# Kernel tuning notes

Hardware: AMD Instinct MI355X
Metric: run time of the kernel (lower is better)

Reference implementation:

```python
import jax, jax.numpy as jnp
import numpy as np

B, T, D, H = 4, 2048, 1024, 16
HD = D // H  # head_dim = 64

def setup_inputs() -> dict:
    key = jax.random.key(0)
    k1, k2, k3 = jax.random.split(key, 3)
    s = 1.0 / np.sqrt(D)
    return {
        "x": jax.random.normal(k1, (B, T, D), dtype=jnp.float32),
        "w_qkv": jax.random.normal(k2, (D, 3 * D), dtype=jnp.float32) * s,
        "b_qkv": jnp.zeros((3 * D,), dtype=jnp.float32),
        "w_proj": jax.random.normal(k3, (D, D), dtype=jnp.float32) * s,
        "b_proj": jnp.zeros((D,), dtype=jnp.float32),
    }

def reference(x, w_qkv, b_qkv, w_proj, b_proj):
    b, t, c = x.shape
    qkv = x @ w_qkv + b_qkv                       # [B,T,3D]
    qkv = qkv.reshape(b, t, 3, H, HD)
    q, k, v = (jnp.transpose(qkv[:, :, i], (0, 2, 1, 3)) for i in range(3))  # [B,H,T,HD]
    scale = 1.0 / np.sqrt(HD)
    attn = jnp.einsum('bhqd,bhkd->bhqk', q, k) * scale  # [B,H,T,T]
    attn = jax.nn.softmax(attn, axis=-1)
    out = jnp.einsum('bhqk,bhkd->bhqd', attn, v)        # [B,H,T,HD]
    out = jnp.transpose(out, (0, 2, 1, 3)).reshape(b, t, c)
    return out @ w_proj + b_proj
```

## Files before the change

### kernel.cpp

```cpp
#include <hip/hip_runtime.h>
#include <hip/hip_bf16.h>

#define T_SEQ   2048
#define D_MODEL 1024
#define N_HEADS 16
#define HEAD_DIM 64
#define BT      8192
#define N3D     3072

using short8  = __attribute__((ext_vector_type(8))) short;
using short4v = __attribute__((ext_vector_type(4))) short;
using floatx4 = __attribute__((ext_vector_type(4))) float;

#define QSCALE 0.18033688f

__device__ __forceinline__ unsigned short rne_bf16(float f) {
  unsigned int u = __float_as_uint(f);
  u = (u + 0x7fffu + ((u >> 16) & 1u)) >> 16;
  return (unsigned short)u;
}

__device__ __forceinline__ void gload_lds16(const unsigned short* g,
                                            unsigned short* l) {
  __builtin_amdgcn_global_load_lds(
      (const __attribute__((address_space(1))) void*)g,
      (__attribute__((address_space(3))) void*)l, 16, 0, 0);
}

__global__ __launch_bounds__(256) void k_convert(const float* __restrict__ in,
                                                 unsigned short* __restrict__ out) {
  size_t i = ((size_t)blockIdx.x * 256 + threadIdx.x) * 8;
  float4 a = *(const float4*)(in + i);
  float4 b = *(const float4*)(in + i + 4);
  short8 v;
  v[0] = (short)rne_bf16(a.x); v[1] = (short)rne_bf16(a.y);
  v[2] = (short)rne_bf16(a.z); v[3] = (short)rne_bf16(a.w);
  v[4] = (short)rne_bf16(b.x); v[5] = (short)rne_bf16(b.y);
  v[6] = (short)rne_bf16(b.z); v[7] = (short)rne_bf16(b.w);
  *(short8*)(((short*)out) + i) = v;
}

__global__ __launch_bounds__(256) void k_transpose_convert(
    const float* __restrict__ in, unsigned short* __restrict__ out_hi,
    int R, int C) {
  __shared__ float tile[64][65];
  int tiles_c = C >> 6;
  int r0 = (blockIdx.x / tiles_c) << 6;
  int c0 = (blockIdx.x % tiles_c) << 6;
  int tid = threadIdx.x;
#pragma unroll
  for (int i = 0; i < 16; ++i) {
    int idx = tid + i * 256;
    int r = idx >> 6, c = idx & 63;
    tile[r][c] = in[(size_t)(r0 + r) * C + c0 + c];
  }
  __syncthreads();
#pragma unroll
  for (int i = 0; i < 16; ++i) {
    int idx = tid + i * 256;
    int orow = idx >> 6, oc = idx & 63;
    out_hi[(size_t)(c0 + orow) * R + r0 + oc] = rne_bf16(tile[oc][orow]);
  }
}

__global__ __launch_bounds__(256) void k_qkv_gemm(
    const unsigned short* __restrict__ A, const unsigned short* __restrict__ Bt,
    const float* __restrict__ bias,
    unsigned short* __restrict__ Qo, unsigned short* __restrict__ Ko,
    unsigned short* __restrict__ Vt) {
  __shared__ __align__(16) unsigned short As[128 * 64];
  __shared__ __align__(16) unsigned short Bs[128 * 64];
  int tid = threadIdx.x;
  int wg = (blockIdx.x & 7) * 192 + (blockIdx.x >> 3);
  int m0 = (wg / 24) * 128;
  int n0 = (wg % 24) * 128;
  int which = n0 >> 10;
  int w = tid >> 6, lane = tid & 63, quad = lane >> 4, l16 = lane & 15;
  int wm = (w >> 1) * 64, wn = (w & 1) * 64;
  floatx4 acc[4][4] = {};

  int r0 = tid >> 3;
  int gsh = (((tid & 7) ^ (r0 & 7)) << 3);

  int a_off[4][2], b_off[4][2];
#pragma unroll
  for (int t = 0; t < 4; ++t) {
    int ra = wm + t * 16 + l16, rb = wn + t * 16 + l16;
#pragma unroll
    for (int ks = 0; ks < 2; ++ks) {
      a_off[t][ks] = ra * 64 + (((ks * 4 + quad) ^ (ra & 7)) << 3);
      b_off[t][ks] = rb * 64 + (((ks * 4 + quad) ^ (rb & 7)) << 3);
    }
  }

  for (int k0 = 0; k0 < 1024; k0 += 64) {
#pragma unroll
    for (int i = 0; i < 4; ++i) {
      int sub = (tid & ~63) + i * 256;
      gload_lds16(A + (size_t)(m0 + r0 + i * 32) * 1024 + k0 + gsh,
                  &As[sub * 8]);
      gload_lds16(Bt + (size_t)(n0 + r0 + i * 32) * 1024 + k0 + gsh,
                  &Bs[sub * 8]);
    }
    __syncthreads();
#pragma unroll
    for (int ks = 0; ks < 2; ++ks) {
      short8 af[4], bfr[4];
#pragma unroll
      for (int mt = 0; mt < 4; ++mt) af[mt] = *(const short8*)(&As[a_off[mt][ks]]);
#pragma unroll
      for (int nt = 0; nt < 4; ++nt) bfr[nt] = *(const short8*)(&Bs[b_off[nt][ks]]);
      if (which == 2) {
#pragma unroll
        for (int mt = 0; mt < 4; ++mt)
#pragma unroll
          for (int nt = 0; nt < 4; ++nt)
            acc[mt][nt] = __builtin_amdgcn_mfma_f32_16x16x32_bf16(af[mt], bfr[nt],
                                                                  acc[mt][nt], 0, 0, 0);
      } else {
#pragma unroll
        for (int mt = 0; mt < 4; ++mt)
#pragma unroll
          for (int nt = 0; nt < 4; ++nt)
            acc[mt][nt] = __builtin_amdgcn_mfma_f32_16x16x32_bf16(bfr[nt], af[mt],
                                                                  acc[mt][nt], 0, 0, 0);
      }
    }
    __syncthreads();
  }

  if (which == 2) {
#pragma unroll
    for (int nt = 0; nt < 4; ++nt) {
      int n = n0 + wn + nt * 16 + l16;
      float bv = bias[n];
      int nn = n & 1023;
      int h = nn >> 6, hd = nn & 63;
#pragma unroll
      for (int mt = 0; mt < 4; ++mt) {
        int mbase = m0 + wm + mt * 16 + quad * 4;
        int b = mbase >> 11;
        int t0 = mbase & 2047;
        int head = b * N_HEADS + h;
        short4v vv;
#pragma unroll
        for (int r = 0; r < 4; ++r) vv[r] = (short)rne_bf16(acc[mt][nt][r] + bv);
        *(short4v*)(&Vt[((size_t)head * HEAD_DIM + hd) * T_SEQ + t0]) = vv;
      }
    }
  } else {
    unsigned short* dst = (which == 0) ? Qo : Ko;
    float scl = (which == 0) ? QSCALE : 1.0f;
#pragma unroll
    for (int nt = 0; nt < 4; ++nt) {
      int nbase = n0 + wn + nt * 16 + quad * 4;
      int nn = nbase & 1023;
      int h = nn >> 6, hd0 = nn & 63;
      float4 bv4 = *(const float4*)(&bias[nbase]);
#pragma unroll
      for (int mt = 0; mt < 4; ++mt) {
        int m = m0 + wm + mt * 16 + l16;
        int b = m >> 11;
        int t = m & 2047;
        int head = b * N_HEADS + h;
        short4v ov;
        ov[0] = (short)rne_bf16((acc[mt][nt][0] + bv4.x) * scl);
        ov[1] = (short)rne_bf16((acc[mt][nt][1] + bv4.y) * scl);
        ov[2] = (short)rne_bf16((acc[mt][nt][2] + bv4.z) * scl);
        ov[3] = (short)rne_bf16((acc[mt][nt][3] + bv4.w) * scl);
        *(short4v*)(&dst[((size_t)head * T_SEQ + t) * HEAD_DIM + hd0]) = ov;
      }
    }
  }
}

__global__ __launch_bounds__(512, 4) void k_attn(
    const unsigned short* __restrict__ Q, const unsigned short* __restrict__ K,
    const unsigned short* __restrict__ Vt, unsigned short* __restrict__ Oo) {
  __shared__ __align__(16) unsigned short Klds[2][64 * 64];
  __shared__ __align__(16) unsigned short Vlds[3][64 * 64];
  int tid = threadIdx.x;
  int head = ((blockIdx.x & 7) << 3) + (blockIdx.x >> 6);
  int qb = ((blockIdx.x >> 3) & 7) << 8;
  int b = head >> 4, h = head & 15;
  int w = tid >> 6, lane = tid & 63, quad = lane >> 4, l16 = lane & 15;
  const unsigned short* Qh = Q + (size_t)head * T_SEQ * HEAD_DIM;
  const unsigned short* Kh = K + (size_t)head * T_SEQ * HEAD_DIM;
  const unsigned short* Vh = Vt + (size_t)head * HEAD_DIM * T_SEQ;

  short8 qf[2][2];
#pragma unroll
  for (int qi = 0; qi < 2; ++qi) {
    int qrow = qb + w * 32 + qi * 16 + l16;
#pragma unroll
    for (int ks = 0; ks < 2; ++ks)
      qf[qi][ks] = *(const short8*)(Qh + (size_t)qrow * 64 + ks * 32 + quad * 8);
  }

  short8 ones;
#pragma unroll
  for (int j = 0; j < 8; ++j) ones[j] = (short)0x3F80;

  floatx4 O[2][4] = {};
  floatx4 Osum[2] = {};
  const floatx4 zf = {};

  int sg = tid >> 6;
  int xs = lane ^ sg;
  int ntp = xs >> 4, mp = xs & 15;
  int ksrc = ((ntp >> 1) << 5) + ((mp >> 2) << 3) + ((ntp & 1) << 2) + (mp & 3);
  int vsrc = xs;
  int sub = tid & ~63;

  int pu[2][4];
#pragma unroll
  for (int ks = 0; ks < 2; ++ks) {
    int gk = ks * 4 + quad;
#pragma unroll
    for (int t = 0; t < 4; ++t)
      pu[ks][t] = (((gk << 6) + t * 16 + l16) ^ gk) << 3;
  }

  auto stageK = [&](unsigned short* dst, int kb) {
    gload_lds16(Kh + ((size_t)(kb * 64 + ksrc)) * 64 + sg * 8, dst + sub * 8);
  };
  auto stageV = [&](unsigned short* dst, int kb) {
    gload_lds16(Vh + (size_t)vsrc * T_SEQ + kb * 64 + sg * 8, dst + sub * 8);
  };

  short8 pPrev[2][2];

  auto qk = [&](const unsigned short* Kb_, floatx4 (&s)[2][4]) {
#pragma unroll
    for (int ks = 0; ks < 2; ++ks) {
#pragma unroll
      for (int nt = 0; nt < 4; ++nt) {
        short8 kf = *(const short8*)(Kb_ + pu[ks][nt]);
        if (ks == 0) {
          s[0][nt] = __builtin_amdgcn_mfma_f32_16x16x32_bf16(kf, qf[0][0], zf, 0, 0, 0);
          s[1][nt] = __builtin_amdgcn_mfma_f32_16x16x32_bf16(kf, qf[1][0], zf, 0, 0, 0);
        } else {
          s[0][nt] = __builtin_amdgcn_mfma_f32_16x16x32_bf16(kf, qf[0][1], s[0][nt], 0, 0, 0);
          s[1][nt] = __builtin_amdgcn_mfma_f32_16x16x32_bf16(kf, qf[1][1], s[1][nt], 0, 0, 0);
        }
      }
    }
  };

  auto pv = [&](const unsigned short* Vb_) {
#pragma unroll
    for (int ks = 0; ks < 2; ++ks) {
      Osum[0] = __builtin_amdgcn_mfma_f32_16x16x32_bf16(ones, pPrev[0][ks], Osum[0], 0, 0, 0);
      Osum[1] = __builtin_amdgcn_mfma_f32_16x16x32_bf16(ones, pPrev[1][ks], Osum[1], 0, 0, 0);
#pragma unroll
      for (int dt = 0; dt < 4; ++dt) {
        short8 vf = *(const short8*)(Vb_ + pu[ks][dt]);
        O[0][dt] = __builtin_amdgcn_mfma_f32_16x16x32_bf16(vf, pPrev[0][ks], O[0][dt], 0, 0, 0);
        O[1][dt] = __builtin_amdgcn_mfma_f32_16x16x32_bf16(vf, pPrev[1][ks], O[1][dt], 0, 0, 0);
      }
    }
  };

  auto expPack = [&](floatx4 (&s)[2][4]) {
#pragma unroll
    for (int qi = 0; qi < 2; ++qi) {
      unsigned int dw[4][2];
#pragma unroll
      for (int nt = 0; nt < 4; ++nt) {
        float p0 = __builtin_amdgcn_exp2f(s[qi][nt][0]);
        float p1 = __builtin_amdgcn_exp2f(s[qi][nt][1]);
        float p2 = __builtin_amdgcn_exp2f(s[qi][nt][2]);
        float p3 = __builtin_amdgcn_exp2f(s[qi][nt][3]);
        __hip_bfloat162 lo2 = __float22bfloat162_rn(make_float2(p0, p1));
        __hip_bfloat162 hi2 = __float22bfloat162_rn(make_float2(p2, p3));
        dw[nt][0] = *(unsigned int*)&lo2;
        dw[nt][1] = *(unsigned int*)&hi2;
      }
#pragma unroll
      for (int ks = 0; ks < 2; ++ks) {
        union { unsigned int u[4]; short8 s8; } cv;
        cv.u[0] = dw[2 * ks][0];
        cv.u[1] = dw[2 * ks][1];
        cv.u[2] = dw[2 * ks + 1][0];
        cv.u[3] = dw[2 * ks + 1][1];
        pPrev[qi][ks] = cv.s8;
      }
    }
  };

  unsigned short* Kcur = &Klds[1][0];
  unsigned short* Koth = &Klds[0][0];
  unsigned short* Vp = &Vlds[0][0];
  unsigned short* Vc = &Vlds[1][0];
  unsigned short* Vn = &Vlds[2][0];

  stageK(Koth, 0); stageV(Vp, 0);
  __syncthreads();
  stageK(Kcur, 1); stageV(Vc, 1);
  {
    floatx4 s[2][4];
    qk(Koth, s);
    expPack(s);
  }
  __syncthreads();

#pragma unroll 1
  for (int t = 1; t < 32; ++t) {
    if (t < 31) { stageK(Koth, t + 1); stageV(Vn, t + 1); }
    floatx4 s[2][4];
    __builtin_amdgcn_s_setprio(1);
    qk(Kcur, s);
    pv(Vp);
    __builtin_amdgcn_s_setprio(0);
    expPack(s);
    __syncthreads();
    unsigned short* tk = Kcur; Kcur = Koth; Koth = tk;
    unsigned short* tv = Vp; Vp = Vc; Vc = Vn; Vn = tv;
  }
  pv(Vp);

#pragma unroll
  for (int qi = 0; qi < 2; ++qi) {
    float inv = 1.0f / Osum[qi][0];
    int t = qb + w * 32 + qi * 16 + l16;
    size_t rowo = ((size_t)(b * T_SEQ + t)) * D_MODEL + h * HEAD_DIM;
#pragma unroll
    for (int dt = 0; dt < 4; ++dt) {
      short4v ov;
#pragma unroll
      for (int r = 0; r < 4; ++r) ov[r] = (short)rne_bf16(O[qi][dt][r] * inv);
      *(short4v*)(&Oo[rowo + dt * 16 + quad * 4]) = ov;
    }
  }
}

__global__ __launch_bounds__(256) void k_proj_gemm(
    const unsigned short* __restrict__ A, const unsigned short* __restrict__ Bt,
    const float* __restrict__ bias, float* __restrict__ out) {
  __shared__ __align__(16) unsigned short As[128 * 64];
  __shared__ __align__(16) unsigned short Bs[128 * 64];
  int tid = threadIdx.x;
  int wg = (blockIdx.x & 7) * 64 + (blockIdx.x >> 3);
  int m0 = (wg >> 3) * 128;
  int n0 = (wg & 7) * 128;
  int w = tid >> 6, lane = tid & 63, quad = lane >> 4, l16 = lane & 15;
  int wm = (w >> 1) * 64, wn = (w & 1) * 64;
  floatx4 acc[4][4] = {};

  int r0 = tid >> 3;
  int gsh = (((tid & 7) ^ (r0 & 7)) << 3);

  int a_off[4][2], b_off[4][2];
#pragma unroll
  for (int t = 0; t < 4; ++t) {
    int ra = wm + t * 16 + l16, rb = wn + t * 16 + l16;
#pragma unroll
    for (int ks = 0; ks < 2; ++ks) {
      a_off[t][ks] = ra * 64 + (((ks * 4 + quad) ^ (ra & 7)) << 3);
      b_off[t][ks] = rb * 64 + (((ks * 4 + quad) ^ (rb & 7)) << 3);
    }
  }

  for (int k0 = 0; k0 < 1024; k0 += 64) {
#pragma unroll
    for (int i = 0; i < 4; ++i) {
      int sub = (tid & ~63) + i * 256;
      gload_lds16(A + (size_t)(m0 + r0 + i * 32) * 1024 + k0 + gsh,
                  &As[sub * 8]);
      gload_lds16(Bt + (size_t)(n0 + r0 + i * 32) * 1024 + k0 + gsh,
                  &Bs[sub * 8]);
    }
    __syncthreads();
#pragma unroll
    for (int ks = 0; ks < 2; ++ks) {
      short8 af[4], bfr[4];
#pragma unroll
      for (int mt = 0; mt < 4; ++mt) af[mt] = *(const short8*)(&As[a_off[mt][ks]]);
#pragma unroll
      for (int nt = 0; nt < 4; ++nt) bfr[nt] = *(const short8*)(&Bs[b_off[nt][ks]]);
#pragma unroll
      for (int mt = 0; mt < 4; ++mt)
#pragma unroll
        for (int nt = 0; nt < 4; ++nt)
          acc[mt][nt] = __builtin_amdgcn_mfma_f32_16x16x32_bf16(af[mt], bfr[nt],
                                                                acc[mt][nt], 0, 0, 0);
    }
    __syncthreads();
  }

#pragma unroll
  for (int nt = 0; nt < 4; ++nt) {
    int n = n0 + wn + nt * 16 + l16;
    float bv = bias[n];
#pragma unroll
    for (int mt = 0; mt < 4; ++mt)
#pragma unroll
      for (int r = 0; r < 4; ++r) {
        int m = m0 + wm + mt * 16 + quad * 4 + r;
        out[(size_t)m * 1024 + n] = acc[mt][nt][r] + bv;
      }
  }
}

extern "C" void kernel_launch(void* const* d_in, const int* in_sizes, int n_in,
                              void* d_out, int out_size, void* d_ws, size_t ws_size,
                              hipStream_t stream) {
  const float* x     = (const float*)d_in[0];
  const float* wqkv  = (const float*)d_in[1];
  const float* bqkv  = (const float*)d_in[2];
  const float* wproj = (const float*)d_in[3];
  const float* bproj = (const float*)d_in[4];

  char* ws = (char*)d_ws;
  size_t off = 0;
  unsigned short* x_bf  = (unsigned short*)(ws + off); off += (size_t)BT * D_MODEL * 2;
  unsigned short* wq_T  = (unsigned short*)(ws + off); off += (size_t)N3D * D_MODEL * 2;
  unsigned short* wp_T  = (unsigned short*)(ws + off); off += (size_t)D_MODEL * D_MODEL * 2;
  unsigned short* Qb    = (unsigned short*)(ws + off); off += (size_t)BT * D_MODEL * 2;
  unsigned short* Kb    = (unsigned short*)(ws + off); off += (size_t)BT * D_MODEL * 2;
  unsigned short* Vt    = (unsigned short*)(ws + off); off += (size_t)BT * D_MODEL * 2;
  unsigned short* a_bf  = (unsigned short*)(ws + off); off += (size_t)BT * D_MODEL * 2;

  k_convert<<<(BT * D_MODEL) / (256 * 8), 256, 0, stream>>>(x, x_bf);
  k_transpose_convert<<<(1024 / 64) * (3072 / 64), 256, 0, stream>>>(wqkv, wq_T, 1024, 3072);
  k_transpose_convert<<<(1024 / 64) * (1024 / 64), 256, 0, stream>>>(wproj, wp_T, 1024, 1024);
  k_qkv_gemm<<<(BT / 128) * (N3D / 128), 256, 0, stream>>>(x_bf, wq_T, bqkv, Qb, Kb, Vt);
  k_attn<<<512, 512, 0, stream>>>(Qb, Kb, Vt, a_bf);
  k_proj_gemm<<<(BT / 128) * (D_MODEL / 128), 256, 0, stream>>>(a_bf, wp_T, bproj, (float*)d_out);
}
```

Measured before the change: 280.0 us.

## Rewrite QKV and projection GEMMs as 256x256 tiles with double-buffered LDS pipeline

Both GEMM kernels move from 128x128 tiles with 4 waves to 256x256 tiles with 8 waves. Each K step is split into four quadrant sub-steps that interleave direct global-to-LDS loads for the next tiles with MFMA work, and the LDS tiles are double-buffered with explicit vmcnt waits and sched barriers. MFMA sections are raised in priority with setprio, and the projection epilogue now writes float4 rows instead of scalar stores. The aim is to hide memory latency and raise data reuse per tile. In exchange it uses 128KB of LDS per block and launches far fewer blocks (128 for the projection), which may underfill the GPU's compute units.

After: 299.8 us. 7.0% more time.

```diff
diff --git a/kernel.cpp b/kernel.cpp
--- a/kernel.cpp
+++ b/kernel.cpp
@@ -25,6 +25,12 @@
   __builtin_amdgcn_global_load_lds(
       (const __attribute__((address_space(1))) void*)g,
       (__attribute__((address_space(3))) void*)l, 16, 0, 0);
+}
+
+__device__ __forceinline__ void wg_barrier() {
+  __builtin_amdgcn_sched_barrier(0);
+  __builtin_amdgcn_s_barrier();
+  __builtin_amdgcn_sched_barrier(0);
 }
 
 __global__ __launch_bounds__(256) void k_convert(const float* __restrict__ in,
@@ -63,82 +69,145 @@
   }
 }
 
-__global__ __launch_bounds__(256) void k_qkv_gemm(
+__global__ __launch_bounds__(512) void k_qkv_gemm(
     const unsigned short* __restrict__ A, const unsigned short* __restrict__ Bt,
     const float* __restrict__ bias,
     unsigned short* __restrict__ Qo, unsigned short* __restrict__ Ko,
     unsigned short* __restrict__ Vt) {
-  __shared__ __align__(16) unsigned short As[128 * 64];
-  __shared__ __align__(16) unsigned short Bs[128 * 64];
+  __shared__ __align__(16) unsigned short As[2][256 * 64];
+  __shared__ __align__(16) unsigned short Bs[2][256 * 64];
   int tid = threadIdx.x;
-  int wg = (blockIdx.x & 7) * 192 + (blockIdx.x >> 3);
-  int m0 = (wg / 24) * 128;
-  int n0 = (wg % 24) * 128;
+  int wg = (blockIdx.x & 7) * 48 + (blockIdx.x >> 3);
+  int m0 = (wg / 12) * 256;
+  int n0 = (wg % 12) * 256;
   int which = n0 >> 10;
-  int w = tid >> 6, lane = tid & 63, quad = lane >> 4, l16 = lane & 15;
-  int wm = (w >> 1) * 64, wn = (w & 1) * 64;
-  floatx4 acc[4][4] = {};
+  int lane = tid & 63, quad = lane >> 4, l16 = lane & 15;
+  int w = tid >> 6, wm = w >> 2, wn = w & 3;
+  floatx4 acc[8][4] = {};
 
   int r0 = tid >> 3;
-  int gsh = (((tid & 7) ^ (r0 & 7)) << 3);
-
-  int a_off[4][2], b_off[4][2];
-#pragma unroll
-  for (int t = 0; t < 4; ++t) {
-    int ra = wm + t * 16 + l16, rb = wn + t * 16 + l16;
-#pragma unroll
-    for (int ks = 0; ks < 2; ++ks) {
-      a_off[t][ks] = ra * 64 + (((ks * 4 + quad) ^ (ra & 7)) << 3);
-      b_off[t][ks] = rb * 64 + (((ks * 4 + quad) ^ (rb & 7)) << 3);
-    }
-  }
-
-  for (int k0 = 0; k0 < 1024; k0 += 64) {
-#pragma unroll
-    for (int i = 0; i < 4; ++i) {
-      int sub = (tid & ~63) + i * 256;
-      gload_lds16(A + (size_t)(m0 + r0 + i * 32) * 1024 + k0 + gsh,
-                  &As[sub * 8]);
-      gload_lds16(Bt + (size_t)(n0 + r0 + i * 32) * 1024 + k0 + gsh,
-                  &Bs[sub * 8]);
-    }
-    __syncthreads();
-#pragma unroll
-    for (int ks = 0; ks < 2; ++ks) {
-      short8 af[4], bfr[4];
-#pragma unroll
-      for (int mt = 0; mt < 4; ++mt) af[mt] = *(const short8*)(&As[a_off[mt][ks]]);
-#pragma unroll
-      for (int nt = 0; nt < 4; ++nt) bfr[nt] = *(const short8*)(&Bs[b_off[nt][ks]]);
-      if (which == 2) {
-#pragma unroll
-        for (int mt = 0; mt < 4; ++mt)
-#pragma unroll
-          for (int nt = 0; nt < 4; ++nt)
-            acc[mt][nt] = __builtin_amdgcn_mfma_f32_16x16x32_bf16(af[mt], bfr[nt],
-                                                                  acc[mt][nt], 0, 0, 0);
-      } else {
-#pragma unroll
-        for (int mt = 0; mt < 4; ++mt)
-#pragma unroll
-          for (int nt = 0; nt < 4; ++nt)
-            acc[mt][nt] = __builtin_amdgcn_mfma_f32_16x16x32_bf16(bfr[nt], af[mt],
-                                                                  acc[mt][nt], 0, 0, 0);
-      }
-    }
-    __syncthreads();
+  int gsh = ((tid & 7) ^ (r0 & 7)) << 3;
+  int subsh = (tid & ~63) * 8;
+
+  int a_off[8][2], b_off[4][2];
+#pragma unroll
+  for (int mt = 0; mt < 8; ++mt) {
+    int ra = wm * 128 + mt * 16 + l16;
+#pragma unroll
+    for (int ks = 0; ks < 2; ++ks)
+      a_off[mt][ks] = ra * 64 + (((ks * 4 + quad) ^ (ra & 7)) << 3);
+  }
+#pragma unroll
+  for (int nt = 0; nt < 4; ++nt) {
+    int rb = wn * 64 + nt * 16 + l16;
+#pragma unroll
+    for (int ks = 0; ks < 2; ++ks)
+      b_off[nt][ks] = rb * 64 + (((ks * 4 + quad) ^ (rb & 7)) << 3);
+  }
+
+  auto stA = [&](int buf, int h, int kt) {
+    const unsigned short* s = A + (size_t)(m0 + h * 128 + r0) * 1024 + kt * 64 + gsh;
+    gload_lds16(s,             &As[buf][h * 8192 + subsh]);
+    gload_lds16(s + 64 * 1024, &As[buf][h * 8192 + subsh + 4096]);
+  };
+  auto stB = [&](int buf, int h, int kt) {
+    const unsigned short* s = Bt + (size_t)(n0 + h * 128 + r0) * 1024 + kt * 64 + gsh;
+    gload_lds16(s,             &Bs[buf][h * 8192 + subsh]);
+    gload_lds16(s + 64 * 1024, &Bs[buf][h * 8192 + subsh + 4096]);
+  };
+
+  short8 a[4][2], b0[2][2], b1[2][2];
+  auto ldA = [&](int buf, int qm) {
+#pragma unroll
+    for (int m = 0; m < 4; ++m)
+#pragma unroll
+      for (int k = 0; k < 2; ++k)
+        a[m][k] = *(const short8*)(&As[buf][a_off[qm * 4 + m][k]]);
+  };
+  auto ldB = [&](int buf, int qn, short8 (&b)[2][2]) {
+#pragma unroll
+    for (int n = 0; n < 2; ++n)
+#pragma unroll
+      for (int k = 0; k < 2; ++k)
+        b[n][k] = *(const short8*)(&Bs[buf][b_off[qn * 2 + n][k]]);
+  };
+  auto mm = [&](int qm, int qn, short8 (&b)[2][2]) {
+    __builtin_amdgcn_s_setprio(1);
+    if (which == 2) {
+#pragma unroll
+      for (int m = 0; m < 4; ++m)
+#pragma unroll
+        for (int n = 0; n < 2; ++n)
+#pragma unroll
+          for (int k = 0; k < 2; ++k)
+            acc[qm * 4 + m][qn * 2 + n] = __builtin_amdgcn_mfma_f32_16x16x32_bf16(
+                a[m][k], b[n][k], acc[qm * 4 + m][qn * 2 + n], 0, 0, 0);
+    } else {
+#pragma unroll
+      for (int m = 0; m < 4; ++m)
+#pragma unroll
+        for (int n = 0; n < 2; ++n)
+#pragma unroll
+          for (int k = 0; k < 2; ++k)
+            acc[qm * 4 + m][qn * 2 + n] = __builtin_amdgcn_mfma_f32_16x16x32_bf16(
+                b[n][k], a[m][k], acc[qm * 4 + m][qn * 2 + n], 0, 0, 0);
+    }
+    __builtin_amdgcn_s_setprio(0);
+  };
+
+  stA(0, 0, 0); stB(0, 0, 0); stA(0, 1, 0); stB(0, 1, 0);
+  stB(1, 0, 1); stA(1, 0, 1); stA(1, 1, 1);
+  asm volatile("s_waitcnt vmcnt(6)" ::: "memory");
+  wg_barrier();
+
+#pragma unroll 1
+  for (int t = 0; t < 14; ++t) {
+    int c = t & 1;
+    ldA(c, 0); ldB(c, 0, b0);
+    stB(c ^ 1, 1, t + 1);
+    wg_barrier(); mm(0, 0, b0); wg_barrier();
+    ldB(c, 1, b1);
+    wg_barrier(); mm(0, 1, b1); wg_barrier();
+    ldA(c, 1);
+    stB(c, 0, t + 2);
+    wg_barrier(); mm(1, 1, b1); wg_barrier();
+    stA(c, 0, t + 2); stA(c, 1, t + 2);
+    wg_barrier(); mm(1, 0, b0);
+    asm volatile("s_waitcnt vmcnt(6)" ::: "memory");
+    wg_barrier();
+  }
+  {
+    ldA(0, 0); ldB(0, 0, b0);
+    stB(1, 1, 15);
+    wg_barrier(); mm(0, 0, b0); wg_barrier();
+    ldB(0, 1, b1);
+    wg_barrier(); mm(0, 1, b1); wg_barrier();
+    ldA(0, 1);
+    wg_barrier(); mm(1, 1, b1); wg_barrier();
+    wg_barrier(); mm(1, 0, b0);
+    asm volatile("s_waitcnt vmcnt(0)" ::: "memory");
+    wg_barrier();
+  }
+  {
+    ldA(1, 0); ldB(1, 0, b0);
+    wg_barrier(); mm(0, 0, b0); wg_barrier();
+    ldB(1, 1, b1);
+    wg_barrier(); mm(0, 1, b1); wg_barrier();
+    ldA(1, 1);
+    wg_barrier(); mm(1, 1, b1); wg_barrier();
+    wg_barrier(); mm(1, 0, b0);
   }
 
   if (which == 2) {
 #pragma unroll
     for (int nt = 0; nt < 4; ++nt) {
-      int n = n0 + wn + nt * 16 + l16;
+      int n = n0 + wn * 64 + nt * 16 + l16;
       float bv = bias[n];
       int nn = n & 1023;
       int h = nn >> 6, hd = nn & 63;
 #pragma unroll
-      for (int mt = 0; mt < 4; ++mt) {
-        int mbase = m0 + wm + mt * 16 + quad * 4;
+      for (int mt = 0; mt < 8; ++mt) {
+        int mbase = m0 + wm * 128 + mt * 16 + quad * 4;
         int b = mbase >> 11;
         int t0 = mbase & 2047;
         int head = b * N_HEADS + h;
@@ -153,13 +222,13 @@
     float scl = (which == 0) ? QSCALE : 1.0f;
 #pragma unroll
     for (int nt = 0; nt < 4; ++nt) {
-      int nbase = n0 + wn + nt * 16 + quad * 4;
+      int nbase = n0 + wn * 64 + nt * 16 + quad * 4;
       int nn = nbase & 1023;
       int h = nn >> 6, hd0 = nn & 63;
       float4 bv4 = *(const float4*)(&bias[nbase]);
 #pragma unroll
-      for (int mt = 0; mt < 4; ++mt) {
-        int m = m0 + wm + mt * 16 + l16;
+      for (int mt = 0; mt < 8; ++mt) {
+        int m = m0 + wm * 128 + mt * 16 + l16;
         int b = m >> 11;
         int t = m & 2047;
         int head = b * N_HEADS + h;
@@ -334,71 +403,135 @@
   }
 }
 
-__global__ __launch_bounds__(256) void k_proj_gemm(
+__global__ __launch_bounds__(512) void k_proj_gemm(
     const unsigned short* __restrict__ A, const unsigned short* __restrict__ Bt,
     const float* __restrict__ bias, float* __restrict__ out) {
-  __shared__ __align__(16) unsigned short As[128 * 64];
-  __shared__ __align__(16) unsigned short Bs[128 * 64];
+  __shared__ __align__(16) unsigned short As[2][256 * 64];
+  __shared__ __align__(16) unsigned short Bs[2][256 * 64];
   int tid = threadIdx.x;
-  int wg = (blockIdx.x & 7) * 64 + (blockIdx.x >> 3);
-  int m0 = (wg >> 3) * 128;
-  int n0 = (wg & 7) * 128;
-  int w = tid >> 6, lane = tid & 63, quad = lane >> 4, l16 = lane & 15;
-  int wm = (w >> 1) * 64, wn = (w & 1) * 64;
-  floatx4 acc[4][4] = {};
+  int wg = (blockIdx.x & 7) * 16 + (blockIdx.x >> 3);
+  int m0 = (wg >> 2) * 256;
+  int n0 = (wg & 3) * 256;
+  int lane = tid & 63, quad = lane >> 4, l16 = lane & 15;
+  int w = tid >> 6, wm = w >> 2, wn = w & 3;
+  floatx4 acc[8][4] = {};
 
   int r0 = tid >> 3;
-  int gsh = (((tid & 7) ^ (r0 & 7)) << 3);
-
-  int a_off[4][2], b_off[4][2];
-#pragma unroll
-  for (int t = 0; t < 4; ++t) {
-    int ra = wm + t * 16 + l16, rb = wn + t * 16 + l16;
-#pragma unroll
-    for (int ks = 0; ks < 2; ++ks) {
-      a_off[t][ks] = ra * 64 + (((ks * 4 + quad) ^ (ra & 7)) << 3);
-      b_off[t][ks] = rb * 64 + (((ks * 4 + quad) ^ (rb & 7)) << 3);
-    }
-  }
-
-  for (int k0 = 0; k0 < 1024; k0 += 64) {
-#pragma unroll
-    for (int i = 0; i < 4; ++i) {
-      int sub = (tid & ~63) + i * 256;
-      gload_lds16(A + (size_t)(m0 + r0 + i * 32) * 1024 + k0 + gsh,
-                  &As[sub * 8]);
-      gload_lds16(Bt + (size_t)(n0 + r0 + i * 32) * 1024 + k0 + gsh,
-                  &Bs[sub * 8]);
-    }
-    __syncthreads();
-#pragma unroll
-    for (int ks = 0; ks < 2; ++ks) {
-      short8 af[4], bfr[4];
-#pragma unroll
-      for (int mt = 0; mt < 4; ++mt) af[mt] = *(const short8*)(&As[a_off[mt][ks]]);
-#pragma unroll
-      for (int nt = 0; nt < 4; ++nt) bfr[nt] = *(const short8*)(&Bs[b_off[nt][ks]]);
-#pragma unroll
-      for (int mt = 0; mt < 4; ++mt)
-#pragma unroll
-        for (int nt = 0; nt < 4; ++nt)
-          acc[mt][nt] = __builtin_amdgcn_mfma_f32_16x16x32_bf16(af[mt], bfr[nt],
-                                                                acc[mt][nt], 0, 0, 0);
-    }
-    __syncthreads();
-  }
-
+  int gsh = ((tid & 7) ^ (r0 & 7)) << 3;
+  int subsh = (tid & ~63) * 8;
+
+  int a_off[8][2], b_off[4][2];
+#pragma unroll
+  for (int mt = 0; mt < 8; ++mt) {
+    int ra = wm * 128 + mt * 16 + l16;
+#pragma unroll
+    for (int ks = 0; ks < 2; ++ks)
+      a_off[mt][ks] = ra * 64 + (((ks * 4 + quad) ^ (ra & 7)) << 3);
+  }
 #pragma unroll
   for (int nt = 0; nt < 4; ++nt) {
-    int n = n0 + wn + nt * 16 + l16;
-    float bv = bias[n];
-#pragma unroll
-    for (int mt = 0; mt < 4; ++mt)
-#pragma unroll
-      for (int r = 0; r < 4; ++r) {
-        int m = m0 + wm + mt * 16 + quad * 4 + r;
-        out[(size_t)m * 1024 + n] = acc[mt][nt][r] + bv;
-      }
+    int rb = wn * 64 + nt * 16 + l16;
+#pragma unroll
+    for (int ks = 0; ks < 2; ++ks)
+      b_off[nt][ks] = rb * 64 + (((ks * 4 + quad) ^ (rb & 7)) << 3);
+  }
+
+  auto stA = [&](int buf, int h, int kt) {
+    const unsigned short* s = A + (size_t)(m0 + h * 128 + r0) * 1024 + kt * 64 + gsh;
+    gload_lds16(s,             &As[buf][h * 8192 + subsh]);
+    gload_lds16(s + 64 * 1024, &As[buf][h * 8192 + subsh + 4096]);
+  };
+  auto stB = [&](int buf, int h, int kt) {
+    const unsigned short* s = Bt + (size_t)(n0 + h * 128 + r0) * 1024 + kt * 64 + gsh;
+    gload_lds16(s,             &Bs[buf][h * 8192 + subsh]);
+    gload_lds16(s + 64 * 1024, &Bs[buf][h * 8192 + subsh + 4096]);
+  };
+
+  short8 a[4][2], b0[2][2], b1[2][2];
+  auto ldA = [&](int buf, int qm) {
+#pragma unroll
+    for (int m = 0; m < 4; ++m)
+#pragma unroll
+      for (int k = 0; k < 2; ++k)
+        a[m][k] = *(const short8*)(&As[buf][a_off[qm * 4 + m][k]]);
+  };
+  auto ldB = [&](int buf, int qn, short8 (&b)[2][2]) {
+#pragma unroll
+    for (int n = 0; n < 2; ++n)
+#pragma unroll
+      for (int k = 0; k < 2; ++k)
+        b[n][k] = *(const short8*)(&Bs[buf][b_off[qn * 2 + n][k]]);
+  };
+  auto mm = [&](int qm, int qn, short8 (&b)[2][2]) {
+    __builtin_amdgcn_s_setprio(1);
+#pragma unroll
+    for (int m = 0; m < 4; ++m)
+#pragma unroll
+      for (int n = 0; n < 2; ++n)
+#pragma unroll
+        for (int k = 0; k < 2; ++k)
+          acc[qm * 4 + m][qn * 2 + n] = __builtin_amdgcn_mfma_f32_16x16x32_bf16(
+              b[n][k], a[m][k], acc[qm * 4 + m][qn * 2 + n], 0, 0, 0);
+    __builtin_amdgcn_s_setprio(0);
+  };
+
+  stA(0, 0, 0); stB(0, 0, 0); stA(0, 1, 0); stB(0, 1, 0);
+  stB(1, 0, 1); stA(1, 0, 1); stA(1, 1, 1);
+  asm volatile("s_waitcnt vmcnt(6)" ::: "memory");
+  wg_barrier();
+
+#pragma unroll 1
+  for (int t = 0; t < 14; ++t) {
+    int c = t & 1;
+    ldA(c, 0); ldB(c, 0, b0);
+    stB(c ^ 1, 1, t + 1);
+    wg_barrier(); mm(0, 0, b0); wg_barrier();
+    ldB(c, 1, b1);
+    wg_barrier(); mm(0, 1, b1); wg_barrier();
+    ldA(c, 1);
+    stB(c, 0, t + 2);
+    wg_barrier(); mm(1, 1, b1); wg_barrier();
+    stA(c, 0, t + 2); stA(c, 1, t + 2);
+    wg_barrier(); mm(1, 0, b0);
+    asm volatile("s_waitcnt vmcnt(6)" ::: "memory");
+    wg_barrier();
+  }
+  {
+    ldA(0, 0); ldB(0, 0, b0);
+    stB(1, 1, 15);
+    wg_barrier(); mm(0, 0, b0); wg_barrier();
+    ldB(0, 1, b1);
+    wg_barrier(); mm(0, 1, b1); wg_barrier();
+    ldA(0, 1);
+    wg_barrier(); mm(1, 1, b1); wg_barrier();
+    wg_barrier(); mm(1, 0, b0);
+    asm volatile("s_waitcnt vmcnt(0)" ::: "memory");
+    wg_barrier();
+  }
+  {
+    ldA(1, 0); ldB(1, 0, b0);
+    wg_barrier(); mm(0, 0, b0); wg_barrier();
+    ldB(1, 1, b1);
+    wg_barrier(); mm(0, 1, b1); wg_barrier();
+    ldA(1, 1);
+    wg_barrier(); mm(1, 1, b1); wg_barrier();
+    wg_barrier(); mm(1, 0, b0);
+  }
+
+#pragma unroll
+  for (int nt = 0; nt < 4; ++nt) {
+    int nbase = n0 + wn * 64 + nt * 16 + quad * 4;
+    float4 bv4 = *(const float4*)(&bias[nbase]);
+#pragma unroll
+    for (int mt = 0; mt < 8; ++mt) {
+      int m = m0 + wm * 128 + mt * 16 + l16;
+      float4 o;
+      o.x = acc[mt][nt][0] + bv4.x;
+      o.y = acc[mt][nt][1] + bv4.y;
+      o.z = acc[mt][nt][2] + bv4.z;
+      o.w = acc[mt][nt][3] + bv4.w;
+      *(float4*)(&out[(size_t)m * 1024 + nbase]) = o;
+    }
   }
 }
 
@@ -424,7 +557,7 @@
   k_convert<<<(BT * D_MODEL) / (256 * 8), 256, 0, stream>>>(x, x_bf);
   k_transpose_convert<<<(1024 / 64) * (3072 / 64), 256, 0, stream>>>(wqkv, wq_T, 1024, 3072);
   k_transpose_convert<<<(1024 / 64) * (1024 / 64), 256, 0, stream>>>(wproj, wp_T, 1024, 1024);
-  k_qkv_gemm<<<(BT / 128) * (N3D / 128), 256, 0, stream>>>(x_bf, wq_T, bqkv, Qb, Kb, Vt);
+  k_qkv_gemm<<<384, 512, 0, stream>>>(x_bf, wq_T, bqkv, Qb, Kb, Vt);
   k_attn<<<512, 512, 0, stream>>>(Qb, Kb, Vt, a_bf);
-  k_proj_gemm<<<(BT / 128) * (D_MODEL / 128), 256, 0, stream>>>(a_bf, wp_T, bproj, (float*)d_out);
-}
+  k_proj_gemm<<<128, 512, 0, stream>>>(a_bf, wp_T, bproj, (float*)d_out);
+}
```
